# Kernel optimization log

Hardware: AMD Instinct MI355X
Metric: run time of the kernel (lower is better)

Reference implementation:

```python
import jax, jax.numpy as jnp
import numpy as np
import math

NQ = 6        # n_qubits_data
NL = 2        # n_layers (active_layers == n_layers)
K = 3         # unfold kernel
C = 64        # channels
SD = 128      # style_dim
B, H, W = 8, 64, 64
PD = C * K * K  # patch_dim = 576


def _apply_1q(psi, U, w):
    # psi: [bsz, 2,2,...,2]; U: [2,2] or [bsz,2,2]
    psi = jnp.moveaxis(psi, 1 + w, -1)
    if U.ndim == 2:
        psi = jnp.einsum('...j,ij->...i', psi, U)
    else:
        psi = jnp.einsum('b...j,bij->b...i', psi, U)
    return jnp.moveaxis(psi, -1, 1 + w)


def _ry_mat(theta):
    c = jnp.cos(theta / 2)
    s = jnp.sin(theta / 2)
    m = jnp.stack([jnp.stack([c, -s], -1), jnp.stack([s, c], -1)], -2)
    return m.astype(jnp.complex64)


def _rz_mat(theta):
    t = theta.astype(jnp.complex64)
    em = jnp.exp(-0.5j * t)
    ep = jnp.exp(0.5j * t)
    z = jnp.zeros_like(em)
    return jnp.stack([jnp.stack([em, z], -1), jnp.stack([z, ep], -1)], -2)


def _u3_mat(theta, phi, lam):
    t = theta.astype(jnp.complex64)
    p = phi.astype(jnp.complex64)
    l = lam.astype(jnp.complex64)
    ct = jnp.cos(t / 2)
    st = jnp.sin(t / 2)
    return jnp.stack([
        jnp.stack([ct, -jnp.exp(1j * l) * st], -1),
        jnp.stack([jnp.exp(1j * p) * st, jnp.exp(1j * (p + l)) * ct], -1)
    ], -2)


def _cnot(psi, c, t):
    c0, c1 = jnp.split(psi, 2, axis=1 + c)
    c1 = jnp.flip(c1, axis=1 + t)
    return jnp.concatenate([c0, c1], axis=1 + c)


def _forward(x, style, data_proj_w, data_proj_b, style_to_data_w, style_to_data_b,
             qcnn_rot_params, measure_params, out_proj_w, out_proj_b,
             res_proj_w, res_proj_b):
    Bx, Cx, Hx, Wx = x.shape
    # nn.Unfold(3, padding=1): [B, C*9, H*W], channel-major then kernel pos
    xp = jnp.pad(x, ((0, 0), (0, 0), (1, 1), (1, 1)))
    pats = jnp.stack([xp[:, :, i:i + Hx, j:j + Wx]
                      for i in range(K) for j in range(K)], axis=2)  # [B,C,9,H,W]
    patches_flat = pats.reshape(Bx, Cx * K * K, Hx * Wx).transpose(0, 2, 1).reshape(-1, Cx * K * K)
    style_flat = jnp.broadcast_to(style[:, None, :], (Bx, Hx * Wx, style.shape[-1])).reshape(-1, style.shape[-1])

    data_angles = jnp.tanh(patches_flat @ data_proj_w.T + data_proj_b) * math.pi   # [bsz, NQ]
    style_angles = jnp.tanh(style_flat @ style_to_data_w.T + style_to_data_b) * math.pi

    bsz = patches_flat.shape[0]
    psi = jnp.zeros((bsz,) + (2,) * NQ, jnp.complex64)
    psi = psi.at[(slice(None),) + (0,) * NQ].set(1.0)

    # hybrid encoding: RY(data + style) per wire (batched angles)
    theta0 = data_angles + style_angles
    for i in range(NQ):
        psi = _apply_1q(psi, _ry_mat(theta0[:, i]), i)

    # HEA layers: per-wire RY/RZ (scalar params) + ring CNOTs
    for l in range(NL):
        for i in range(NQ):
            psi = _apply_1q(psi, _ry_mat(qcnn_rot_params[l, i, 0, 0]), i)
            psi = _apply_1q(psi, _rz_mat(qcnn_rot_params[l, i, 1, 0]), i)
        for i in range(NQ):
            psi = _cnot(psi, i, (i + 1) % NQ)

    # trainable measurement basis (U3 per wire)
    for i in range(NQ):
        psi = _apply_1q(psi, _u3_mat(measure_params[i, 0], measure_params[i, 1], measure_params[i, 2]), i)

    # PauliZ expvals on all wires
    probs = psi.real ** 2 + psi.imag ** 2
    expvals = []
    for i in range(NQ):
        p = jnp.sum(probs, axis=tuple(a for a in range(1, NQ + 1) if a != 1 + i))  # [bsz,2]
        expvals.append(p[:, 0] - p[:, 1])
    quant_out = jnp.stack(expvals, -1)  # [bsz, NQ]

    out_flat = (quant_out @ out_proj_w.T + out_proj_b) + (patches_flat @ res_proj_w.T + res_proj_b)
    return out_flat.reshape(Bx, Hx, Wx, -1).transpose(0, 3, 1, 2)


def setup_inputs() -> dict:
    key = jax.random.key(0)
    ks = jax.random.split(key, 10)
    return {
        'x': jax.random.normal(ks[0], (B, C, H, W), jnp.float32),
        'style': jax.random.normal(ks[1], (B, SD), jnp.float32),
        'data_proj_w': jax.random.normal(ks[2], (NQ, PD), jnp.float32) * 0.02,
        'data_proj_b': jnp.zeros((NQ,), jnp.float32),
        'style_to_data_w': jax.random.normal(ks[3], (NQ, SD), jnp.float32) * 0.02,
        'style_to_data_b': jnp.zeros((NQ,), jnp.float32),
        'qcnn_rot_params': jax.random.normal(ks[4], (NL, NQ, 2, 3), jnp.float32) * 0.1,
        'measure_params': jax.random.normal(ks[5], (NQ, 3), jnp.float32) * 0.1,
        'out_proj_w': jax.random.normal(ks[6], (C, NQ), jnp.float32) * 0.02,
        'out_proj_b': jnp.zeros((C,), jnp.float32),
        'res_proj_w': jax.random.normal(ks[7], (C, PD), jnp.float32) * 0.02,
        'res_proj_b': jnp.zeros((C,), jnp.float32),
    }


def reference(x, style, data_proj_w, data_proj_b, style_to_data_w, style_to_data_b,
              qcnn_rot_params, measure_params, out_proj_w, out_proj_b,
              res_proj_w, res_proj_b):
    return _forward(x, style, data_proj_w, data_proj_b, style_to_data_w, style_to_data_b,
                    qcnn_rot_params, measure_params, out_proj_w, out_proj_b,
                    res_proj_w, res_proj_b)
```

## Files before the change

### kernel.cpp

```cpp
#include <hip/hip_runtime.h>
#include <math.h>

#define PI_F 3.14159265358979323846f

typedef __attribute__((ext_vector_type(8))) short bf16x8;
typedef __attribute__((ext_vector_type(4))) float f32x4;

__device__ float g_Ur[64 * 64];
__device__ float g_Ui[64 * 64];
__device__ float g_Zw[64 * 64];
__device__ float g_sang[48];
__device__ float g_cb[64];
__device__ __attribute__((aligned(16))) unsigned short g_Bm[5 * 18 * 64 * 8];

__device__ inline unsigned short bf16rne(float f) {
    unsigned u = __float_as_uint(f);
    return (unsigned short)((u + 0x7FFFu + ((u >> 16) & 1u)) >> 16);
}

__global__ __launch_bounds__(64) void k_prep(
        const float* __restrict__ style,
        const float* __restrict__ dw, const float* __restrict__ rw,
        const float* __restrict__ s2dw, const float* __restrict__ s2db,
        const float* __restrict__ qcnn, const float* __restrict__ meas,
        const float* __restrict__ outw, const float* __restrict__ outb,
        const float* __restrict__ resb) {
    int bid = blockIdx.x;
    int t = threadIdx.x;

    if (bid >= 66) {
        int entry = (bid - 66) * 64 + t;
        int nt   = entry / 1152;
        int rem  = entry - nt * 1152;
        int slab = rem >> 6;
        int ln   = rem & 63;
        int m    = ln & 15, quad = ln >> 4;
        int n    = nt * 16 + m;
        int ij   = slab >> 1;
        int ch   = (slab & 1) * 32;
#pragma unroll
        for (int j = 0; j < 8; ++j) {
            int c = ch + quad * 8 + j;
            int ko = c * 9 + ij;
            float v = 0.f;
            if (n < 64)      v = rw[n * 576 + ko];
            else if (n < 70) v = dw[(n - 64) * 576 + ko];
            g_Bm[entry * 8 + j] = bf16rne(v);
        }
        return;
    }
    if (bid == 0) {
        float zr[6];
#pragma unroll
        for (int q = 0; q < 6; ++q) zr[q] = ((t >> (5 - q)) & 1) ? -1.f : 1.f;
#pragma unroll 8
        for (int c = 0; c < 64; ++c) {
            float z = 0.f;
#pragma unroll
            for (int q = 0; q < 6; ++q) z += outw[c * 6 + q] * zr[q];
            g_Zw[t * 64 + c] = z;
        }
        g_cb[t] = outb[t] + resb[t];
        return;
    }
    if (bid == 1) {
        if (t < 48) {
            int bb = t / 6, q = t % 6;
            float a = s2db[q];
#pragma unroll 8
            for (int j = 0; j < 128; ++j) a += style[bb * 128 + j] * s2dw[q * 128 + j];
            g_sang[t] = tanhf(a) * PI_F;
        }
        return;
    }

    int s = bid - 2;
    float ar = (t == s) ? 1.f : 0.f;
    float ai = 0.f;

#pragma unroll
    for (int l = 0; l < 2; ++l) {
#pragma unroll
        for (int wq = 0; wq < 6; ++wq) {
            int mask = 1 << (5 - wq);
            bool hi = (t & mask) != 0;
            float th = qcnn[((l * 6 + wq) * 2 + 0) * 3];
            float sg, cg; sincosf(0.5f * th, &sg, &cg);
            float pr = __shfl_xor(ar, mask);
            float pi2 = __shfl_xor(ai, mask);
            ar = hi ? (sg * pr + cg * ar) : (cg * ar - sg * pr);
            ai = hi ? (sg * pi2 + cg * ai) : (cg * ai - sg * pi2);
            float ph = qcnn[((l * 6 + wq) * 2 + 1) * 3];
            float sz, cz; sincosf(0.5f * ph, &sz, &cz);
            float szz = hi ? sz : -sz;
            float nr = cz * ar - szz * ai;
            float ni = cz * ai + szz * ar;
            ar = nr; ai = ni;
        }
#pragma unroll
        for (int wq = 0; wq < 6; ++wq) {
            int cm = 1 << (5 - wq);
            int tm = 1 << (5 - ((wq + 1) % 6));
            float pr = __shfl_xor(ar, tm);
            float pi2 = __shfl_xor(ai, tm);
            if (t & cm) { ar = pr; ai = pi2; }
        }
    }
#pragma unroll
    for (int wq = 0; wq < 6; ++wq) {
        int mask = 1 << (5 - wq);
        bool hi = (t & mask) != 0;
        float th = meas[wq * 3 + 0], ph = meas[wq * 3 + 1], lm = meas[wq * 3 + 2];
        float st2, ct; sincosf(0.5f * th, &st2, &ct);
        float sl, cl;  sincosf(lm, &sl, &cl);
        float sp, cp;  sincosf(ph, &sp, &cp);
        float spl, cpl; sincosf(ph + lm, &spl, &cpl);
        float u01r = -cl * st2, u01i = -sl * st2;
        float u10r =  cp * st2, u10i =  sp * st2;
        float u11r =  cpl * ct, u11i =  spl * ct;
        float pr = __shfl_xor(ar, mask);
        float pi2 = __shfl_xor(ai, mask);
        float nr, ni;
        if (hi) {
            nr = u10r * pr - u10i * pi2 + u11r * ar - u11i * ai;
            ni = u10r * pi2 + u10i * pr + u11r * ai + u11i * ar;
        } else {
            nr = ct * ar + u01r * pr - u01i * pi2;
            ni = ct * ai + u01r * pi2 + u01i * pr;
        }
        ar = nr; ai = ni;
    }
    g_Ur[t * 64 + s] = ar;
    g_Ui[t * 64 + s] = ai;
}

__global__ __launch_bounds__(1024, 4) void k_main(const float* __restrict__ x,
                                                  const float* __restrict__ dpb,
                                                  float* __restrict__ out) {
    __shared__ __attribute__((aligned(16))) float smem[13504];
    unsigned*       xsu32 = (unsigned*)smem;
    const unsigned short* xsu = (const unsigned short*)smem;
    float*          convres = smem + 8320;

    int tid  = threadIdx.x;
    int lane = tid & 63;
    int wid  = __builtin_amdgcn_readfirstlane(tid >> 6);
    int m    = lane & 15;
    int quad = lane >> 4;

    int p = blockIdx.x * 64 + lane;
    int b = p >> 12;
    int h = (p >> 6) & 63;
    int w = p & 63;
    const float* xb = x + (b << 18);

    if (tid < 216) {
        int r3 = tid / 72, rest = tid % 72;
        int half = rest / 36, cp = rest % 36;
        xsu32[(r3 * 66 + half * 65) * 36 + cp] = 0u;
    }
#pragma unroll
    for (int k = 0; k < 6; ++k) {
        int flat = k * 1024 + tid;
        int row  = flat >> 11;
        int rem  = flat & 2047;
        int cp   = rem >> 6;
        int w2   = rem & 63;
        int hh   = h + row - 1;
        float v0 = 0.f, v1 = 0.f;
        if ((unsigned)hh < 64u) {
            const float* px = xb + (hh << 6) + w2;
            v0 = px[(2 * cp) << 12];
            v1 = px[(2 * cp + 1) << 12];
        }
        xsu32[(row * 66 + w2 + 1) * 36 + cp] =
            (unsigned)bf16rne(v0) | ((unsigned)bf16rne(v1) << 16);
    }
    __syncthreads();

    int mt0 = wid >> 2, nt0 = wid & 3;
    const unsigned short* a0base = xsu + (mt0 * 16 + m) * 72 + quad * 8;
    const unsigned short* b0base = g_Bm + ((nt0 * 18) * 64 + lane) * 8;
    f32x4 acc0 = {0.f, 0.f, 0.f, 0.f};
    f32x4 acc1 = {0.f, 0.f, 0.f, 0.f};
    if (wid < 4) {
        const unsigned short* a1base = xsu + (wid * 16 + m) * 72 + quad * 8;
        const unsigned short* b1base = g_Bm + ((4 * 18) * 64 + lane) * 8;
#pragma unroll
        for (int slab = 0; slab < 18; ++slab) {
            int ij = slab >> 1, i = ij / 3, j = ij - 3 * (ij / 3);
            int aoff = i * 4752 + j * 72 + (slab & 1) * 32;
            bf16x8 a0 = *(const bf16x8*)(a0base + aoff);
            bf16x8 b0 = *(const bf16x8*)(b0base + slab * 512);
            acc0 = __builtin_amdgcn_mfma_f32_16x16x32_bf16(a0, b0, acc0, 0, 0, 0);
            bf16x8 a1 = *(const bf16x8*)(a1base + aoff);
            bf16x8 b1 = *(const bf16x8*)(b1base + slab * 512);
            acc1 = __builtin_amdgcn_mfma_f32_16x16x32_bf16(a1, b1, acc1, 0, 0, 0);
        }
    } else {
#pragma unroll
        for (int slab = 0; slab < 18; ++slab) {
            int ij = slab >> 1, i = ij / 3, j = ij - 3 * (ij / 3);
            int aoff = i * 4752 + j * 72 + (slab & 1) * 32;
            bf16x8 a0 = *(const bf16x8*)(a0base + aoff);
            bf16x8 b0 = *(const bf16x8*)(b0base + slab * 512);
            acc0 = __builtin_amdgcn_mfma_f32_16x16x32_bf16(a0, b0, acc0, 0, 0, 0);
        }
    }
#pragma unroll
    for (int r = 0; r < 4; ++r) {
        convres[(mt0 * 16 + quad * 4 + r) * 81 + nt0 * 16 + m] = acc0[r];
    }
    if (wid < 4) {
#pragma unroll
        for (int r = 0; r < 4; ++r) {
            convres[(wid * 16 + quad * 4 + r) * 81 + 64 + m] = acc1[r];
        }
    }
    __syncthreads();

    float sc[6], co[6];
#pragma unroll
    for (int q = 0; q < 6; ++q) {
        float t = convres[lane * 81 + 64 + q];
        float theta = tanhf(t + dpb[q]) * PI_F + g_sang[b * 6 + q];
        sincosf(0.5f * theta, &sc[q], &co[q]);
    }

#pragma unroll
    for (int ti = 0; ti < 4; ++ti) {
        int s = wid * 4 + ti;
        float v = ((s >> 5) & 1) ? sc[0] : co[0];
        v *= ((s >> 4) & 1) ? sc[1] : co[1];
        v *= ((s >> 3) & 1) ? sc[2] : co[2];
        v *= ((s >> 2) & 1) ? sc[3] : co[3];
        v *= ((s >> 1) & 1) ? sc[4] : co[4];
        v *= (s & 1)        ? sc[5] : co[5];
        smem[lane * 65 + s] = v;
    }
    __syncthreads();

    int t0 = wid * 4;
    float yr[4], yi[4];
#pragma unroll
    for (int t = 0; t < 4; ++t) { yr[t] = 0.f; yi[t] = 0.f; }
#pragma unroll
    for (int s0 = 0; s0 < 8; ++s0) {
        float ps[8];
#pragma unroll
        for (int k = 0; k < 8; ++k) ps[k] = smem[lane * 65 + s0 * 8 + k];
#pragma unroll
        for (int t = 0; t < 4; ++t) {
            const float4 u0 = *(const float4*)(g_Ur + ((t0 + t) << 6) + s0 * 8);
            const float4 u1 = *(const float4*)(g_Ur + ((t0 + t) << 6) + s0 * 8 + 4);
            const float4 v0 = *(const float4*)(g_Ui + ((t0 + t) << 6) + s0 * 8);
            const float4 v1 = *(const float4*)(g_Ui + ((t0 + t) << 6) + s0 * 8 + 4);
            yr[t] += u0.x * ps[0] + u0.y * ps[1] + u0.z * ps[2] + u0.w * ps[3]
                   + u1.x * ps[4] + u1.y * ps[5] + u1.z * ps[6] + u1.w * ps[7];
            yi[t] += v0.x * ps[0] + v0.y * ps[1] + v0.z * ps[2] + v0.w * ps[3]
                   + v1.x * ps[4] + v1.y * ps[5] + v1.z * ps[6] + v1.w * ps[7];
        }
    }
#pragma unroll
    for (int t = 0; t < 4; ++t)
        smem[4160 + lane * 65 + t0 + t] = yr[t] * yr[t] + yi[t] * yi[t];
    __syncthreads();

    if (wid < 8) {
        int c0 = wid * 8;
        float acc[8];
#pragma unroll
        for (int k = 0; k < 8; ++k) acc[k] = convres[lane * 81 + c0 + k];
#pragma unroll 8
        for (int t = 0; t < 64; ++t) {
            float pr = smem[4160 + lane * 65 + t];
            const float4 z0 = *(const float4*)(g_Zw + (t << 6) + c0);
            const float4 z1 = *(const float4*)(g_Zw + (t << 6) + c0 + 4);
            acc[0] += pr * z0.x; acc[1] += pr * z0.y;
            acc[2] += pr * z0.z; acc[3] += pr * z0.w;
            acc[4] += pr * z1.x; acc[5] += pr * z1.y;
            acc[6] += pr * z1.z; acc[7] += pr * z1.w;
        }
        int ob = (b << 18) + (h << 6) + w;
#pragma unroll
        for (int k = 0; k < 8; ++k) {
            out[ob + ((c0 + k) << 12)] = acc[k] + g_cb[c0 + k];
        }
    }
}

extern "C" void kernel_launch(void* const* d_in, const int* in_sizes, int n_in,
                              void* d_out, int out_size, void* d_ws, size_t ws_size,
                              hipStream_t stream) {
    const float* x     = (const float*)d_in[0];
    const float* style = (const float*)d_in[1];
    const float* dw    = (const float*)d_in[2];
    const float* dpb   = (const float*)d_in[3];
    const float* s2dw  = (const float*)d_in[4];
    const float* s2db  = (const float*)d_in[5];
    const float* qcnn  = (const float*)d_in[6];
    const float* meas  = (const float*)d_in[7];
    const float* outw  = (const float*)d_in[8];
    const float* outb  = (const float*)d_in[9];
    const float* rw    = (const float*)d_in[10];
    const float* resb  = (const float*)d_in[11];
    float* out = (float*)d_out;

    hipLaunchKernelGGL(k_prep, dim3(156), dim3(64), 0, stream,
                       style, dw, rw, s2dw, s2db, qcnn, meas, outw, outb, resb);
    hipLaunchKernelGGL(k_main, dim3(512), dim3(1024), 0, stream, x, dpb, out);
}
```

Baseline: 120.5 us.

## Move quantum unitary and output projection matmuls onto bf16 MFMA

The per-pixel 64x64 complex unitary application and the 64x64 measurement-to-channel projection now run as bf16 MFMA tiles instead of scalar FP32 FMAs reading global float matrices. The unitaries and projection weights are stored in bf16 in prep, and the state amplitudes are built as a product state and packed to bf16 in LDS. Sincos work is spread across six waves, and the output store is reorganized so every wave writes four channels. This cuts scalar ALU work and global matrix traffic, but adds bf16 rounding error to the amplitudes, probabilities and weights, plus extra barriers.

Measured after the change: 109.0 us. 9.5% less time.

```diff
diff --git a/kernel.cpp b/kernel.cpp
--- a/kernel.cpp
+++ b/kernel.cpp
@@ -6,11 +6,11 @@
 typedef __attribute__((ext_vector_type(8))) short bf16x8;
 typedef __attribute__((ext_vector_type(4))) float f32x4;
 
-__device__ float g_Ur[64 * 64];
-__device__ float g_Ui[64 * 64];
-__device__ float g_Zw[64 * 64];
 __device__ float g_sang[48];
 __device__ float g_cb[64];
+__device__ __attribute__((aligned(16))) unsigned short g_Urb[64 * 64];
+__device__ __attribute__((aligned(16))) unsigned short g_Uib[64 * 64];
+__device__ __attribute__((aligned(16))) unsigned short g_Zwc[64 * 64];
 __device__ __attribute__((aligned(16))) unsigned short g_Bm[5 * 18 * 64 * 8];
 
 __device__ inline unsigned short bf16rne(float f) {
@@ -58,7 +58,7 @@
             float z = 0.f;
 #pragma unroll
             for (int q = 0; q < 6; ++q) z += outw[c * 6 + q] * zr[q];
-            g_Zw[t * 64 + c] = z;
+            g_Zwc[c * 64 + t] = bf16rne(z);
         }
         g_cb[t] = outb[t] + resb[t];
         return;
@@ -130,17 +130,20 @@
         }
         ar = nr; ai = ni;
     }
-    g_Ur[t * 64 + s] = ar;
-    g_Ui[t * 64 + s] = ai;
+    g_Urb[t * 64 + s] = bf16rne(ar);
+    g_Uib[t * 64 + s] = bf16rne(ai);
 }
 
 __global__ __launch_bounds__(1024, 4) void k_main(const float* __restrict__ x,
                                                   const float* __restrict__ dpb,
                                                   float* __restrict__ out) {
     __shared__ __attribute__((aligned(16))) float smem[13504];
-    unsigned*       xsu32 = (unsigned*)smem;
-    const unsigned short* xsu = (const unsigned short*)smem;
+    unsigned*             xsu32 = (unsigned*)smem;
+    const unsigned short* xsu   = (const unsigned short*)smem;
     float*          convres = smem + 8320;
+    float*          fact    = smem;
+    unsigned short* psi_bf  = (unsigned short*)(smem + 1024);
+    unsigned short* p_bf    = (unsigned short*)(smem + 3328);
 
     int tid  = threadIdx.x;
     int lane = tid & 63;
@@ -219,73 +222,80 @@
     }
     __syncthreads();
 
-    float sc[6], co[6];
-#pragma unroll
-    for (int q = 0; q < 6; ++q) {
+    if (wid < 6) {
+        int q = wid;
         float t = convres[lane * 81 + 64 + q];
         float theta = tanhf(t + dpb[q]) * PI_F + g_sang[b * 6 + q];
-        sincosf(0.5f * theta, &sc[q], &co[q]);
-    }
-
-#pragma unroll
-    for (int ti = 0; ti < 4; ++ti) {
-        int s = wid * 4 + ti;
-        float v = ((s >> 5) & 1) ? sc[0] : co[0];
-        v *= ((s >> 4) & 1) ? sc[1] : co[1];
-        v *= ((s >> 3) & 1) ? sc[2] : co[2];
-        v *= ((s >> 2) & 1) ? sc[3] : co[3];
-        v *= ((s >> 1) & 1) ? sc[4] : co[4];
-        v *= (s & 1)        ? sc[5] : co[5];
-        smem[lane * 65 + s] = v;
-    }
-    __syncthreads();
-
-    int t0 = wid * 4;
-    float yr[4], yi[4];
-#pragma unroll
-    for (int t = 0; t < 4; ++t) { yr[t] = 0.f; yi[t] = 0.f; }
-#pragma unroll
-    for (int s0 = 0; s0 < 8; ++s0) {
-        float ps[8];
-#pragma unroll
-        for (int k = 0; k < 8; ++k) ps[k] = smem[lane * 65 + s0 * 8 + k];
-#pragma unroll
-        for (int t = 0; t < 4; ++t) {
-            const float4 u0 = *(const float4*)(g_Ur + ((t0 + t) << 6) + s0 * 8);
-            const float4 u1 = *(const float4*)(g_Ur + ((t0 + t) << 6) + s0 * 8 + 4);
-            const float4 v0 = *(const float4*)(g_Ui + ((t0 + t) << 6) + s0 * 8);
-            const float4 v1 = *(const float4*)(g_Ui + ((t0 + t) << 6) + s0 * 8 + 4);
-            yr[t] += u0.x * ps[0] + u0.y * ps[1] + u0.z * ps[2] + u0.w * ps[3]
-                   + u1.x * ps[4] + u1.y * ps[5] + u1.z * ps[6] + u1.w * ps[7];
-            yi[t] += v0.x * ps[0] + v0.y * ps[1] + v0.z * ps[2] + v0.w * ps[3]
-                   + v1.x * ps[4] + v1.y * ps[5] + v1.z * ps[6] + v1.w * ps[7];
-        }
-    }
-#pragma unroll
-    for (int t = 0; t < 4; ++t)
-        smem[4160 + lane * 65 + t0 + t] = yr[t] * yr[t] + yi[t] * yi[t];
-    __syncthreads();
-
-    if (wid < 8) {
-        int c0 = wid * 8;
-        float acc[8];
-#pragma unroll
-        for (int k = 0; k < 8; ++k) acc[k] = convres[lane * 81 + c0 + k];
-#pragma unroll 8
-        for (int t = 0; t < 64; ++t) {
-            float pr = smem[4160 + lane * 65 + t];
-            const float4 z0 = *(const float4*)(g_Zw + (t << 6) + c0);
-            const float4 z1 = *(const float4*)(g_Zw + (t << 6) + c0 + 4);
-            acc[0] += pr * z0.x; acc[1] += pr * z0.y;
-            acc[2] += pr * z0.z; acc[3] += pr * z0.w;
-            acc[4] += pr * z1.x; acc[5] += pr * z1.y;
-            acc[6] += pr * z1.z; acc[7] += pr * z1.w;
-        }
-        int ob = (b << 18) + (h << 6) + w;
-#pragma unroll
-        for (int k = 0; k < 8; ++k) {
-            out[ob + ((c0 + k) << 12)] = acc[k] + g_cb[c0 + k];
-        }
+        float sv, cv; sincosf(0.5f * theta, &sv, &cv);
+        fact[q * 64 + lane] = sv;
+        fact[(6 + q) * 64 + lane] = cv;
+    }
+    __syncthreads();
+
+    {
+        float f0s = fact[0 * 64 + lane], f0c = fact[6 * 64 + lane];
+        float f1s = fact[1 * 64 + lane], f1c = fact[7 * 64 + lane];
+        float f2s = fact[2 * 64 + lane], f2c = fact[8 * 64 + lane];
+        float f3s = fact[3 * 64 + lane], f3c = fact[9 * 64 + lane];
+        float f4s = fact[4 * 64 + lane], f4c = fact[10 * 64 + lane];
+        float f5s = fact[5 * 64 + lane], f5c = fact[11 * 64 + lane];
+        int sb = wid * 4;
+        float pre = (((sb >> 5) & 1) ? f0s : f0c)
+                  * (((sb >> 4) & 1) ? f1s : f1c)
+                  * (((sb >> 3) & 1) ? f2s : f2c)
+                  * (((sb >> 2) & 1) ? f3s : f3c);
+        unsigned short pk[4];
+#pragma unroll
+        for (int ti = 0; ti < 4; ++ti) {
+            float v = pre * ((ti & 2) ? f4s : f4c) * ((ti & 1) ? f5s : f5c);
+            pk[ti] = bf16rne(v);
+        }
+        *(uint2*)(psi_bf + lane * 72 + sb) =
+            make_uint2((unsigned)pk[0] | ((unsigned)pk[1] << 16),
+                       (unsigned)pk[2] | ((unsigned)pk[3] << 16));
+    }
+    __syncthreads();
+
+    {
+        const unsigned short* pa = psi_bf + (mt0 * 16 + m) * 72 + quad * 8;
+        const unsigned short* ur = g_Urb + (nt0 * 16 + m) * 64 + quad * 8;
+        const unsigned short* ui = g_Uib + (nt0 * 16 + m) * 64 + quad * 8;
+        bf16x8 aA = *(const bf16x8*)(pa);
+        bf16x8 aB = *(const bf16x8*)(pa + 32);
+        f32x4 c1 = {0.f, 0.f, 0.f, 0.f};
+        f32x4 c2 = {0.f, 0.f, 0.f, 0.f};
+        c1 = __builtin_amdgcn_mfma_f32_16x16x32_bf16(aA, *(const bf16x8*)(ur), c1, 0, 0, 0);
+        c1 = __builtin_amdgcn_mfma_f32_16x16x32_bf16(aB, *(const bf16x8*)(ur + 32), c1, 0, 0, 0);
+        c2 = __builtin_amdgcn_mfma_f32_16x16x32_bf16(aA, *(const bf16x8*)(ui), c2, 0, 0, 0);
+        c2 = __builtin_amdgcn_mfma_f32_16x16x32_bf16(aB, *(const bf16x8*)(ui + 32), c2, 0, 0, 0);
+#pragma unroll
+        for (int r = 0; r < 4; ++r) {
+            float pv = c1[r] * c1[r] + c2[r] * c2[r];
+            p_bf[(mt0 * 16 + quad * 4 + r) * 72 + nt0 * 16 + m] = bf16rne(pv);
+        }
+    }
+    __syncthreads();
+
+    {
+        const unsigned short* pa = p_bf + (mt0 * 16 + m) * 72 + quad * 8;
+        const unsigned short* zc = g_Zwc + (nt0 * 16 + m) * 64 + quad * 8;
+        f32x4 o = {0.f, 0.f, 0.f, 0.f};
+        o = __builtin_amdgcn_mfma_f32_16x16x32_bf16(*(const bf16x8*)(pa),
+                                                    *(const bf16x8*)(zc), o, 0, 0, 0);
+        o = __builtin_amdgcn_mfma_f32_16x16x32_bf16(*(const bf16x8*)(pa + 32),
+                                                    *(const bf16x8*)(zc + 32), o, 0, 0, 0);
+#pragma unroll
+        for (int r = 0; r < 4; ++r) {
+            convres[(mt0 * 16 + quad * 4 + r) * 81 + nt0 * 16 + m] += o[r];
+        }
+    }
+    __syncthreads();
+
+    int ob = (b << 18) + (h << 6) + w;
+#pragma unroll
+    for (int kk = 0; kk < 4; ++kk) {
+        int c = wid * 4 + kk;
+        out[ob + (c << 12)] = convres[lane * 81 + c] + g_cb[c];
     }
 }
 
```
